# Optimization experiments

Measured on AMD Instinct MI355X. Metric: run time of the kernel, lower is better.

## Reference

```python
import jax, jax.numpy as jnp
import numpy as np

INTEGRAL_RESOLUTION = 0.03  # matches self.integral_resolution

S, H, E, G, F = 4096, 3, 512, 3334, 1  # samples, heads, max events, grid points, formulas


def setup_inputs() -> dict:
    key = jax.random.key(0)
    k1, k2, k3, k4, k5, k6 = jax.random.split(key, 6)
    event_features = jax.random.uniform(k1, (S, H, E, F), dtype=jnp.float32)
    event_mask = jax.random.randint(k2, (S, H, E), 0, 2).astype(bool)
    grid_features = jax.random.uniform(k3, (S, H, G, F), dtype=jnp.float32)
    weights = jax.random.normal(k4, (H, F), dtype=jnp.float32)
    bases = jax.random.normal(k5, (H,), dtype=jnp.float32)
    effects = jnp.ones((H, F), dtype=jnp.float32)  # formula effect is +/-1
    return {
        "event_features": event_features,
        "event_mask": event_mask,
        "grid_features": grid_features,
        "weights": weights,
        "bases": bases,
        "effects": effects,
    }


def reference(event_features, event_mask, grid_features, weights, bases, effects):
    # intensity(t, h) = exp(base_h + sum_f w_{h,f} * feature_f(t) * effect_{h,f})
    w_eff = weights * effects  # [H, F]
    # log-intensity at event times: [S, H, E]
    ev_logit = bases[None, :, None] + jnp.einsum('shef,hf->she', event_features, w_eff)
    # log-intensity on the integral grid: [S, H, G]
    gr_logit = bases[None, :, None] + jnp.einsum('shgf,hf->shg', grid_features, w_eff)
    # sum of log(intensity) over valid events (log(exp(x)) = x)
    log_sum = jnp.sum(jnp.where(event_mask, ev_logit, jnp.zeros((), ev_logit.dtype)))
    # Riemann integral of intensity over [0, T_max]
    integral = jnp.asarray(INTEGRAL_RESOLUTION, gr_logit.dtype) * jnp.sum(jnp.exp(gr_logit))
    return log_sum - integral
```

## Files before the change

### kernel.cpp

```cpp
#include <hip/hip_runtime.h>

constexpr int S = 4096;
constexpr int H = 3;
constexpr int E = 512;
constexpr int G = 3334;
constexpr float RES = 0.03f;
constexpr float LOG2E = 1.44269504088896340736f;

constexpr int NBLK = 2048;
constexpr int BT   = 256;
constexpr int NF4G = S * H * G / 4;
constexpr int GPB  = NF4G / NBLK;
constexpr int NF4E = S * H * E / 4;
constexpr int EPB  = NF4E / NBLK;
constexpr int TAIL_T = GPB - 19 * BT;

#if __has_builtin(__builtin_amdgcn_exp2f)
#define EXP2(x) __builtin_amdgcn_exp2f(x)
#else
#define EXP2(x) exp2f(x)
#endif

__device__ __forceinline__ float quad_exp(int fidx, float4 y,
                                          float c0, float c1, float c2,
                                          float v0, float v1, float v2) {
    int j = fidx * 4;
    int q = j / G;
    int r = j - q * G;
    int m = q - (q / 3) * 3;
    int hB = (m == 2) ? 0 : (m + 1);
    float cA = (m == 0) ? c0 : ((m == 1) ? c1 : c2);
    float vA = (m == 0) ? v0 : ((m == 1) ? v1 : v2);
    float cB = (hB == 0) ? c0 : ((hB == 1) ? c1 : c2);
    float vB = (hB == 0) ? v0 : ((hB == 1) ? v1 : v2);
    int lim = G - r;
    float s;
    s  = EXP2(cA + vA * y.x);
    s += EXP2(((1 >= lim) ? cB : cA) + ((1 >= lim) ? vB : vA) * y.y);
    s += EXP2(((2 >= lim) ? cB : cA) + ((2 >= lim) ? vB : vA) * y.z);
    s += EXP2(((3 >= lim) ? cB : cA) + ((3 >= lim) ? vB : vA) * y.w);
    return s;
}

__global__ __launch_bounds__(256) void logic_model_kernel(
    const float* __restrict__ ev,
    const int*   __restrict__ mask,
    const float* __restrict__ gr,
    const float* __restrict__ w,
    const float* __restrict__ bases,
    const float* __restrict__ eff,
    float* __restrict__ out)
{
    const float b0 = bases[0], b1 = bases[1], b2 = bases[2];
    const float w0 = w[0] * eff[0], w1 = w[1] * eff[1], w2 = w[2] * eff[2];
    const float c0 = b0 * LOG2E, c1 = b1 * LOG2E, c2 = b2 * LOG2E;
    const float v0 = w0 * LOG2E, v1 = w1 * LOG2E, v2 = w2 * LOG2E;

    const int t = threadIdx.x;
    const float4* ev4 = (const float4*)ev;
    const int4*   m4  = (const int4*)mask;
    const float4* gr4 = (const float4*)gr;

    const int ebase = blockIdx.x * EPB + t;
    const int gbase = blockIdx.x * GPB;

    float4 p1x[3]; int4 p1m[3];
    #pragma unroll
    for (int u = 0; u < 3; ++u) {
        p1x[u] = ev4[ebase + u * BT];
        p1m[u] = m4[ebase + u * BT];
    }
    float4 buf[4][4];
    #pragma unroll
    for (int g = 0; g < 3; ++g) {
        #pragma unroll
        for (int u = 0; u < 4; ++u) {
            int slot = 4 * g + u;
            buf[g][u] = gr4[gbase + t + slot * BT];
        }
    }
    __builtin_amdgcn_sched_barrier(0);

    float acc_ev = 0.f;
    #pragma unroll
    for (int u = 0; u < 3; ++u) {
        int row = (ebase + u * BT) >> 7;
        int h = row - (row / 3) * 3;
        float bb = (h == 0) ? b0 : ((h == 1) ? b1 : b2);
        float ww = (h == 0) ? w0 : ((h == 1) ? w1 : w2);
        float4 x = p1x[u]; int4 m = p1m[u];
        if (m.x) acc_ev += bb + ww * x.x;
        if (m.y) acc_ev += bb + ww * x.y;
        if (m.z) acc_ev += bb + ww * x.z;
        if (m.w) acc_ev += bb + ww * x.w;
    }
    __builtin_amdgcn_sched_barrier(0);

    float acc_gr = 0.f;
    #pragma unroll
    for (int b = 0; b < 5; ++b) {
        if (b + 3 < 5) {
            int g = b + 3;
            #pragma unroll
            for (int u = 0; u < 4; ++u) {
                int slot = 4 * g + u;
                int pos = t + slot * BT;
                int idx = gbase + ((slot == 19 && t >= TAIL_T) ? 0 : pos);
                buf[g & 3][u] = gr4[idx];
            }
        }
        __builtin_amdgcn_sched_barrier(0);
        #pragma unroll
        for (int u = 0; u < 4; ++u) {
            int slot = 4 * b + u;
            int pos = t + slot * BT;
            bool valid = (slot < 19) || (t < TAIL_T);
            int fidx = gbase + (valid ? pos : 0);
            float s = quad_exp(fidx, buf[b & 3][u], c0, c1, c2, v0, v1, v2);
            acc_gr += valid ? s : 0.f;
        }
        __builtin_amdgcn_sched_barrier(0);
    }

    float v = acc_ev - RES * acc_gr;

    #pragma unroll
    for (int off = 32; off > 0; off >>= 1)
        v += __shfl_down(v, off, 64);

    __shared__ float sdata[4];
    const int wave = threadIdx.x >> 6;
    const int lane = threadIdx.x & 63;
    if (lane == 0) sdata[wave] = v;
    __syncthreads();
    if (threadIdx.x == 0) {
        float s = sdata[0] + sdata[1] + sdata[2] + sdata[3];
        atomicAdd(out, s);
    }
}

extern "C" void kernel_launch(void* const* d_in, const int* in_sizes, int n_in,
                              void* d_out, int out_size, void* d_ws, size_t ws_size,
                              hipStream_t stream) {
    const float* ev    = (const float*)d_in[0];
    const int*   mask  = (const int*)  d_in[1];
    const float* gr    = (const float*)d_in[2];
    const float* wgt   = (const float*)d_in[3];
    const float* bases = (const float*)d_in[4];
    const float* eff   = (const float*)d_in[5];
    float* out = (float*)d_out;

    hipMemsetAsync(out, 0, sizeof(float), stream);

    logic_model_kernel<<<NBLK, BT, 0, stream>>>(ev, mask, gr, wgt, bases, eff, out);
}
```

Before: 272.0 us.

## Replace atomic accumulation with per-block partials and a final reduce kernel

Drops the memset and the global atomicAdd. Each block now writes a partial sum to the workspace, and a single-block second kernel reduces the partials deterministically. It also simplifies index math by using block-local grid indices with a cheaper mod-3, derives the head for events from thread position, cuts the prefetch pipeline from 4 to 3 buffers, and switches to exp2f. The extra kernel launch adds a small fixed cost, and the shallower prefetch may expose more memory latency.

```diff
diff --git a/kernel.cpp b/kernel.cpp
--- a/kernel.cpp
+++ b/kernel.cpp
@@ -9,25 +9,19 @@
 
 constexpr int NBLK = 2048;
 constexpr int BT   = 256;
-constexpr int NF4G = S * H * G / 4;
-constexpr int GPB  = NF4G / NBLK;
-constexpr int NF4E = S * H * E / 4;
-constexpr int EPB  = NF4E / NBLK;
+constexpr int GPB  = S * H * G / 4 / NBLK;
+constexpr int EPB  = S * H * E / 4 / NBLK;
 constexpr int TAIL_T = GPB - 19 * BT;
 
-#if __has_builtin(__builtin_amdgcn_exp2f)
-#define EXP2(x) __builtin_amdgcn_exp2f(x)
-#else
-#define EXP2(x) exp2f(x)
-#endif
+typedef float f4_t __attribute__((ext_vector_type(4)));
+typedef int   i4_t __attribute__((ext_vector_type(4)));
 
-__device__ __forceinline__ float quad_exp(int fidx, float4 y,
-                                          float c0, float c1, float c2,
-                                          float v0, float v1, float v2) {
-    int j = fidx * 4;
-    int q = j / G;
-    int r = j - q * G;
-    int m = q - (q / 3) * 3;
+__device__ __forceinline__ float quad_exp2l(int jl, f4_t y,
+                                            float c0, float c1, float c2,
+                                            float v0, float v1, float v2) {
+    int q  = jl / G;
+    int r  = jl - q * G;
+    int m  = (q >= 3) ? (q - 3) : q;
     int hB = (m == 2) ? 0 : (m + 1);
     float cA = (m == 0) ? c0 : ((m == 1) ? c1 : c2);
     float vA = (m == 0) ? v0 : ((m == 1) ? v1 : v2);
@@ -35,10 +29,10 @@
     float vB = (hB == 0) ? v0 : ((hB == 1) ? v1 : v2);
     int lim = G - r;
     float s;
-    s  = EXP2(cA + vA * y.x);
-    s += EXP2(((1 >= lim) ? cB : cA) + ((1 >= lim) ? vB : vA) * y.y);
-    s += EXP2(((2 >= lim) ? cB : cA) + ((2 >= lim) ? vB : vA) * y.z);
-    s += EXP2(((3 >= lim) ? cB : cA) + ((3 >= lim) ? vB : vA) * y.w);
+    s  = exp2f(cA + vA * y.x);
+    s += exp2f(((1 >= lim) ? cB : cA) + ((1 >= lim) ? vB : vA) * y.y);
+    s += exp2f(((2 >= lim) ? cB : cA) + ((2 >= lim) ? vB : vA) * y.z);
+    s += exp2f(((3 >= lim) ? cB : cA) + ((3 >= lim) ? vB : vA) * y.w);
     return s;
 }
 
@@ -49,7 +43,7 @@
     const float* __restrict__ w,
     const float* __restrict__ bases,
     const float* __restrict__ eff,
-    float* __restrict__ out)
+    float* __restrict__ partials)
 {
     const float b0 = bases[0], b1 = bases[1], b2 = bases[2];
     const float w0 = w[0] * eff[0], w1 = w[1] * eff[1], w2 = w[2] * eff[2];
@@ -57,66 +51,66 @@
     const float v0 = w0 * LOG2E, v1 = w1 * LOG2E, v2 = w2 * LOG2E;
 
     const int t = threadIdx.x;
-    const float4* ev4 = (const float4*)ev;
-    const int4*   m4  = (const int4*)mask;
-    const float4* gr4 = (const float4*)gr;
+    const int b = blockIdx.x;
 
-    const int ebase = blockIdx.x * EPB + t;
-    const int gbase = blockIdx.x * GPB;
+    const f4_t* ev4 = (const f4_t*)ev;
+    const i4_t* m4  = (const i4_t*)mask;
+    const f4_t* gr4 = (const f4_t*)gr;
 
-    float4 p1x[3]; int4 p1m[3];
+    const int ebase = b * EPB + t;
+    const int gbase = b * GPB;
+
+    f4_t p1x[3]; i4_t p1m[3];
     #pragma unroll
     for (int u = 0; u < 3; ++u) {
         p1x[u] = ev4[ebase + u * BT];
         p1m[u] = m4[ebase + u * BT];
     }
-    float4 buf[4][4];
+    f4_t buf[3][4];
     #pragma unroll
-    for (int g = 0; g < 3; ++g) {
+    for (int g = 0; g < 2; ++g)
         #pragma unroll
-        for (int u = 0; u < 4; ++u) {
-            int slot = 4 * g + u;
-            buf[g][u] = gr4[gbase + t + slot * BT];
-        }
-    }
+        for (int u = 0; u < 4; ++u)
+            buf[g][u] = gr4[gbase + t + (4 * g + u) * BT];
     __builtin_amdgcn_sched_barrier(0);
 
     float acc_ev = 0.f;
-    #pragma unroll
-    for (int u = 0; u < 3; ++u) {
-        int row = (ebase + u * BT) >> 7;
-        int h = row - (row / 3) * 3;
-        float bb = (h == 0) ? b0 : ((h == 1) ? b1 : b2);
-        float ww = (h == 0) ? w0 : ((h == 1) ? w1 : w2);
-        float4 x = p1x[u]; int4 m = p1m[u];
-        if (m.x) acc_ev += bb + ww * x.x;
-        if (m.y) acc_ev += bb + ww * x.y;
-        if (m.z) acc_ev += bb + ww * x.z;
-        if (m.w) acc_ev += bb + ww * x.w;
+    {
+        const bool hi = (t >= 128);
+        #pragma unroll
+        for (int u = 0; u < 3; ++u) {
+            int h = (u == 0) ? (hi ? 1 : 0) : ((u == 1) ? (hi ? 0 : 2) : (hi ? 2 : 1));
+            float bb = (h == 0) ? b0 : ((h == 1) ? b1 : b2);
+            float ww = (h == 0) ? w0 : ((h == 1) ? w1 : w2);
+            f4_t x = p1x[u]; i4_t m = p1m[u];
+            if (m.x) acc_ev += bb + ww * x.x;
+            if (m.y) acc_ev += bb + ww * x.y;
+            if (m.z) acc_ev += bb + ww * x.z;
+            if (m.w) acc_ev += bb + ww * x.w;
+        }
     }
     __builtin_amdgcn_sched_barrier(0);
 
     float acc_gr = 0.f;
     #pragma unroll
-    for (int b = 0; b < 5; ++b) {
-        if (b + 3 < 5) {
-            int g = b + 3;
+    for (int g = 0; g < 5; ++g) {
+        if (g + 2 < 5) {
             #pragma unroll
             for (int u = 0; u < 4; ++u) {
-                int slot = 4 * g + u;
-                int pos = t + slot * BT;
-                int idx = gbase + ((slot == 19 && t >= TAIL_T) ? 0 : pos);
-                buf[g & 3][u] = gr4[idx];
+                int slot = 4 * (g + 2) + u;
+                int pos  = t + slot * BT;
+                int idx  = gbase + ((slot == 19 && t >= TAIL_T) ? 0 : pos);
+                buf[(g + 2) % 3][u] = gr4[idx];
             }
         }
         __builtin_amdgcn_sched_barrier(0);
         #pragma unroll
         for (int u = 0; u < 4; ++u) {
-            int slot = 4 * b + u;
-            int pos = t + slot * BT;
+            int slot = 4 * g + u;
+            int pos  = t + slot * BT;
             bool valid = (slot < 19) || (t < TAIL_T);
-            int fidx = gbase + (valid ? pos : 0);
-            float s = quad_exp(fidx, buf[b & 3][u], c0, c1, c2, v0, v1, v2);
+            int jl = 4 * (valid ? pos : 0);
+            float s = quad_exp2l(jl, buf[g % 3][u], c0, c1, c2, v0, v1, v2);
             acc_gr += valid ? s : 0.f;
         }
         __builtin_amdgcn_sched_barrier(0);
@@ -129,14 +123,28 @@
         v += __shfl_down(v, off, 64);
 
     __shared__ float sdata[4];
-    const int wave = threadIdx.x >> 6;
-    const int lane = threadIdx.x & 63;
-    if (lane == 0) sdata[wave] = v;
+    if ((t & 63) == 0) sdata[t >> 6] = v;
     __syncthreads();
-    if (threadIdx.x == 0) {
-        float s = sdata[0] + sdata[1] + sdata[2] + sdata[3];
-        atomicAdd(out, s);
-    }
+    if (t == 0)
+        partials[b] = sdata[0] + sdata[1] + sdata[2] + sdata[3];
+}
+
+__global__ __launch_bounds__(256) void reduce_kernel(
+    const float* __restrict__ partials, float* __restrict__ out)
+{
+    const int t = threadIdx.x;
+    float v = 0.f;
+    #pragma unroll
+    for (int k = 0; k < NBLK / BT; ++k)
+        v += partials[t + k * BT];
+    #pragma unroll
+    for (int off = 32; off > 0; off >>= 1)
+        v += __shfl_down(v, off, 64);
+    __shared__ float sdata[4];
+    if ((t & 63) == 0) sdata[t >> 6] = v;
+    __syncthreads();
+    if (t == 0)
+        out[0] = sdata[0] + sdata[1] + sdata[2] + sdata[3];
 }
 
 extern "C" void kernel_launch(void* const* d_in, const int* in_sizes, int n_in,
@@ -149,8 +157,9 @@
     const float* bases = (const float*)d_in[4];
     const float* eff   = (const float*)d_in[5];
     float* out = (float*)d_out;
+    float* partials = (float*)d_ws;
 
-    hipMemsetAsync(out, 0, sizeof(float), stream);
-
-    logic_model_kernel<<<NBLK, BT, 0, stream>>>(ev, mask, gr, wgt, bases, eff, out);
+    logic_model_kernel<<<NBLK, BT, 0, stream>>>(ev, mask, gr, wgt, bases, eff,
+                                                partials);
+    reduce_kernel<<<1, BT, 0, stream>>>(partials, out);
 }
```

Result: no change. 273.5 us (+0.5%).
